# Kernel optimization log

Measured on AMD Instinct MI355X. Metric: run time of the kernel, lower is better.

Reference implementation:

```python
import jax, jax.numpy as jnp
import numpy as np

N_NODES = 100000
N_EDGES = 3200000
C, H, F = 512, 256, 64


def spmm(edge_row, edge_col, edge_val, Z):
    # (A @ Z)[i] = sum over edges e with row[e]==i of val[e] * Z[col[e]]
    msgs = edge_val[:, None] * Z[edge_col]  # [E, d]
    return jax.ops.segment_sum(msgs, edge_row, num_segments=N_NODES)


def setup_inputs() -> dict:
    key = jax.random.key(0)
    k1, k2, k3, k4, k5, k6, k7 = jax.random.split(key, 7)
    X = jax.random.normal(k1, (N_NODES, C), dtype=jnp.float32)
    edge_row = jax.random.randint(k2, (N_EDGES,), 0, N_NODES, dtype=jnp.int32)
    edge_col = jax.random.randint(k3, (N_EDGES,), 0, N_NODES, dtype=jnp.int32)
    edge_val = jax.random.uniform(k4, (N_EDGES,), dtype=jnp.float32)
    W0 = jax.random.normal(k5, (C, H), dtype=jnp.float32) * (C ** -0.5)
    Wh1 = jax.random.normal(k6, (H, H), dtype=jnp.float32) * (H ** -0.5)
    W1 = jax.random.normal(k7, (H, F), dtype=jnp.float32) * (H ** -0.5)
    return {"X": X, "edge_row": edge_row, "edge_col": edge_col,
            "edge_val": edge_val, "W0": W0, "Wh1": Wh1, "W1": W1}


def reference(X, edge_row, edge_col, edge_val, W0, Wh1, W1):
    # layer 0: relu(A @ (X W0))   (dropout=0 -> identity)
    Z = jax.nn.relu(spmm(edge_row, edge_col, edge_val, X @ W0))
    # hidden layers (num_layers - 2 = 1)
    Z = jax.nn.relu(spmm(edge_row, edge_col, edge_val, Z @ Wh1))
    # output layer: softmax(A @ (Z W1), axis=-1)
    Z = jax.nn.softmax(spmm(edge_row, edge_col, edge_val, Z @ W1), axis=-1)
    return Z
```

## Files before the change

### kernel.cpp

```cpp
#include <hip/hip_runtime.h>
#include <cstdint>
#include <cstddef>


#define SCAN_B 1024

typedef __attribute__((ext_vector_type(8))) short short8_t;
typedef __attribute__((ext_vector_type(4))) short short4_t;
typedef __attribute__((ext_vector_type(4))) float f32x4;

__device__ __forceinline__ short bf16_hi(float x) {
    union { float f; unsigned u; } c; c.f = x;
    return (short)(c.u >> 16);
}
__device__ __forceinline__ float bf16_f32(short h) {
    union { float f; unsigned u; } c; c.u = ((unsigned)(unsigned short)h) << 16;
    return c.f;
}

__device__ __forceinline__ void gload_lds16(const void* g, void* l) {
    __builtin_amdgcn_global_load_lds(
        (const __attribute__((address_space(1))) void*)g,
        (__attribute__((address_space(3))) void*)l, 16, 0, 0);
}


__global__ void count_rows_k(const int* __restrict__ row, int* __restrict__ deg, int E) {
    int e = blockIdx.x * blockDim.x + threadIdx.x;
    if (e < E) atomicAdd(&deg[row[e]], 1);
}

__global__ __launch_bounds__(SCAN_B) void scan1_k(const int* __restrict__ deg,
                                                  int* __restrict__ part,
                                                  int* __restrict__ bsum, int n) {
    __shared__ int buf[SCAN_B];
    int tid = threadIdx.x;
    int i = blockIdx.x * SCAN_B + tid;
    int v = (i < n) ? ((deg[i] + 3) & ~3) : 0;
    buf[tid] = v;
    __syncthreads();
    for (int off = 1; off < SCAN_B; off <<= 1) {
        int y = (tid >= off) ? buf[tid - off] : 0;
        __syncthreads();
        buf[tid] += y;
        __syncthreads();
    }
    if (i < n) part[i] = buf[tid] - v;
    if (tid == SCAN_B - 1) bsum[blockIdx.x] = buf[tid];
}

__global__ __launch_bounds__(128) void scan2_k(int* __restrict__ bsum, int nb) {
    __shared__ int buf[128];
    int tid = threadIdx.x;
    int v = (tid < nb) ? bsum[tid] : 0;
    buf[tid] = v;
    __syncthreads();
    for (int off = 1; off < 128; off <<= 1) {
        int y = (tid >= off) ? buf[tid - off] : 0;
        __syncthreads();
        buf[tid] += y;
        __syncthreads();
    }
    if (tid < nb) bsum[tid] = buf[tid] - v;
    if (tid == nb - 1) bsum[nb] = buf[tid];
}

__global__ __launch_bounds__(SCAN_B) void scan3_k(int* __restrict__ rowptr,
                                                  const int* __restrict__ bsum,
                                                  int* __restrict__ cursor, int n, int nb) {
    int i = blockIdx.x * SCAN_B + threadIdx.x;
    if (i < n) {
        int v = rowptr[i] + bsum[blockIdx.x];
        rowptr[i] = v;
        cursor[i] = v;
    }
    if (i == 0) rowptr[n] = bsum[nb];
}

__global__ void scatter_k(const int* __restrict__ row, const int* __restrict__ col,
                          const float* __restrict__ val, int* __restrict__ cursor,
                          int2* __restrict__ ecv, int E) {
    int e = blockIdx.x * blockDim.x + threadIdx.x;
    if (e < E) {
        int r = row[e];
        int p = atomicAdd(&cursor[r], 1);
        ecv[p] = make_int2(col[e], __float_as_int(val[e]));
    }
}


__global__ void split_w_k(const float* __restrict__ W, short* __restrict__ Bhl,
                          int K, int M) {
    int i = blockIdx.x * 256 + threadIdx.x;
    if (i >= K * M) return;
    int k = i / M, m = i - k * M;
    float x = W[i];
    short hi = bf16_hi(x);
    float r = x - bf16_f32(hi);
    short lo = bf16_hi(r);
    int g = k >> 3, j = k & 7;
    Bhl[(size_t)m * (2 * K) + 16 * g + j] = hi;
    Bhl[(size_t)m * (2 * K) + 16 * g + 8 + j] = lo;
}


template <int K, int BN, int NWR, int NWC, bool AF32>
__global__ __launch_bounds__(256) void gemm_hl(const void* __restrict__ Av,
                                               const short* __restrict__ Bhl,
                                               short* __restrict__ ZQ,
                                               float* __restrict__ scl, int N) {
    constexpr int BM = 64 * NWR;
    constexpr int NF = BN / NWC / 16;
    __shared__ short Ald[BM * 64];
    __shared__ short Bld[BN * 64];

    const int tid = threadIdx.x, lane = tid & 63, w = tid >> 6;
    const int wr = w / NWC, wc = w % NWC;
    const int row0 = blockIdx.x * BM;
    const int l8 = lane >> 3;
    const int sx = (lane & 7) ^ l8;

    f32x4 acc[4][NF] = {};

    for (int k0 = 0; k0 < K; k0 += 32) {
        if constexpr (AF32) {
            const float* A = (const float*)Av;
            int row = tid >> 2, q = tid & 3;
            int gr = row0 + row;
            float4 x0 = make_float4(0.f, 0.f, 0.f, 0.f), x1 = x0;
            if (gr < N) {
                x0 = *(const float4*)&A[(size_t)gr * K + k0 + q * 8];
                x1 = *(const float4*)&A[(size_t)gr * K + k0 + q * 8 + 4];
            }
            float f[8] = {x0.x, x0.y, x0.z, x0.w, x1.x, x1.y, x1.z, x1.w};
            short8_t hi, lo;
#pragma unroll
            for (int j = 0; j < 8; ++j) {
                short hh = bf16_hi(f[j]);
                hi[j] = hh;
                lo[j] = bf16_hi(f[j] - bf16_f32(hh));
            }
            int key = row & 7;
            *(short8_t*)&Ald[row * 64 + ((2 * q) ^ key) * 8] = hi;
            *(short8_t*)&Ald[row * 64 + ((2 * q + 1) ^ key) * 8] = lo;
        } else {
            const short* Ahl = (const short*)Av;
            for (int ch = w; ch < BM / 8; ch += 4)
                gload_lds16(Ahl + (size_t)(row0 + ch * 8 + l8) * (2 * K) + 2 * k0 + sx * 8,
                            &Ald[ch * 512]);
        }
        for (int ch = w; ch < BN / 8; ch += 4)
            gload_lds16(Bhl + (size_t)(ch * 8 + l8) * (2 * K) + 2 * k0 + sx * 8,
                        &Bld[ch * 512]);
        __syncthreads();

        const int sH = (lane >> 4) * 2, sL = sH + 1;
        short8_t ah[4], al[4];
#pragma unroll
        for (int m = 0; m < 4; ++m) {
            int rl = wr * 64 + m * 16 + (lane & 15);
            int key = rl & 7;
            ah[m] = *(const short8_t*)&Ald[rl * 64 + (sH ^ key) * 8];
            al[m] = *(const short8_t*)&Ald[rl * 64 + (sL ^ key) * 8];
        }
#pragma unroll
        for (int n = 0; n < NF; ++n) {
            int cl = wc * (BN / NWC) + n * 16 + (lane & 15);
            int key = cl & 7;
            short8_t bh = *(const short8_t*)&Bld[cl * 64 + (sH ^ key) * 8];
            short8_t bl = *(const short8_t*)&Bld[cl * 64 + (sL ^ key) * 8];
#pragma unroll
            for (int m = 0; m < 4; ++m) {
                acc[m][n] = __builtin_amdgcn_mfma_f32_16x16x32_bf16(ah[m], bh, acc[m][n], 0, 0, 0);
                acc[m][n] = __builtin_amdgcn_mfma_f32_16x16x32_bf16(ah[m], bl, acc[m][n], 0, 0, 0);
                acc[m][n] = __builtin_amdgcn_mfma_f32_16x16x32_bf16(al[m], bh, acc[m][n], 0, 0, 0);
            }
        }
        __syncthreads();
    }

    const int lg = lane >> 4, lc = lane & 15;
    float* maxb = (float*)Ald;
    float rmax[4][4];
#pragma unroll
    for (int m = 0; m < 4; ++m)
#pragma unroll
        for (int r = 0; r < 4; ++r) {
            float v = 0.f;
#pragma unroll
            for (int n = 0; n < NF; ++n) v = fmaxf(v, fabsf(acc[m][n][r]));
#pragma unroll
            for (int o = 8; o >= 1; o >>= 1) v = fmaxf(v, __shfl_xor(v, o));
            rmax[m][r] = v;
        }
    if constexpr (NWC > 1) {
        if (lc == 0)
#pragma unroll
            for (int m = 0; m < 4; ++m)
#pragma unroll
                for (int r = 0; r < 4; ++r)
                    maxb[(wr * 64 + m * 16 + lg * 4 + r) * NWC + wc] = rmax[m][r];
        __syncthreads();
    }
#pragma unroll
    for (int m = 0; m < 4; ++m)
#pragma unroll
        for (int r = 0; r < 4; ++r) {
            int rl = wr * 64 + m * 16 + lg * 4 + r;
            float v = rmax[m][r];
            if constexpr (NWC > 1) {
                v = maxb[rl * NWC];
#pragma unroll
                for (int q = 1; q < NWC; ++q) v = fmaxf(v, maxb[rl * NWC + q]);
            }
            int grow = row0 + rl;
            if (grow < N) {
                float inv = (v > 0.f) ? 32767.f / v : 0.f;
                if (lc == 0 && wc == 0) scl[grow] = v * (1.f / 32767.f);
#pragma unroll
                for (int n = 0; n < NF; ++n)
                    ZQ[(size_t)grow * BN + wc * (BN / NWC) + n * 16 + lc] =
                        (short)rintf(acc[m][n][r] * inv);
            }
        }
}


__global__ __launch_bounds__(256) void spmm_agg256_k(const int* __restrict__ rowptr,
                                                     const int2* __restrict__ ecv,
                                                     const short* __restrict__ Q,
                                                     const float* __restrict__ scl,
                                                     short* __restrict__ Zhl, int N) {
    int row = blockIdx.x * 4 + (threadIdx.x >> 6);
    if (row >= N) return;
    int lane = threadIdx.x & 63;
    int s = rowptr[row], e = rowptr[row + 1];
    const short4_t* Qv = (const short4_t*)Q;
    f32x4 acc = {0.f, 0.f, 0.f, 0.f};
    for (int i = s; i < e; i += 4) {
        int4 a = *(const int4*)(ecv + i);
        int4 b = *(const int4*)(ecv + i + 2);
        float w0 = __int_as_float(a.y) * scl[a.x];
        float w1 = __int_as_float(a.w) * scl[a.z];
        float w2 = __int_as_float(b.y) * scl[b.x];
        float w3 = __int_as_float(b.w) * scl[b.z];
        short4_t q0 = Qv[(size_t)a.x * 64 + lane];
        short4_t q1 = Qv[(size_t)a.z * 64 + lane];
        short4_t q2 = Qv[(size_t)b.x * 64 + lane];
        short4_t q3 = Qv[(size_t)b.z * 64 + lane];
#pragma unroll
        for (int j = 0; j < 4; ++j) {
            acc[j] = fmaf(w0, (float)q0[j], acc[j]);
            acc[j] = fmaf(w1, (float)q1[j], acc[j]);
            acc[j] = fmaf(w2, (float)q2[j], acc[j]);
            acc[j] = fmaf(w3, (float)q3[j], acc[j]);
        }
    }
    short4_t hi, lo;
#pragma unroll
    for (int j = 0; j < 4; ++j) {
        float r = fmaxf(acc[j], 0.f);
        short h = bf16_hi(r);
        hi[j] = h;
        lo[j] = bf16_hi(r - bf16_f32(h));
    }
    size_t base = (size_t)row * 512 + (lane >> 1) * 16 + (lane & 1) * 4;
    *(short4_t*)&Zhl[base] = hi;
    *(short4_t*)&Zhl[base + 8] = lo;
}

__global__ __launch_bounds__(256) void spmm_softmax64_k(const int* __restrict__ rowptr,
                                                        const int2* __restrict__ ecv,
                                                        const short* __restrict__ Q,
                                                        const float* __restrict__ scl,
                                                        float* __restrict__ out, int N) {
    int row = blockIdx.x * 4 + (threadIdx.x >> 6);
    if (row >= N) return;
    int lane = threadIdx.x & 63;
    int s = rowptr[row], e = rowptr[row + 1];
    float acc = 0.f;
    for (int i = s; i < e; i += 4) {
        int4 a = *(const int4*)(ecv + i);
        int4 b = *(const int4*)(ecv + i + 2);
        float w0 = __int_as_float(a.y) * scl[a.x];
        float w1 = __int_as_float(a.w) * scl[a.z];
        float w2 = __int_as_float(b.y) * scl[b.x];
        float w3 = __int_as_float(b.w) * scl[b.z];
        float z0 = (float)Q[(size_t)a.x * 64 + lane];
        float z1 = (float)Q[(size_t)a.z * 64 + lane];
        float z2 = (float)Q[(size_t)b.x * 64 + lane];
        float z3 = (float)Q[(size_t)b.z * 64 + lane];
        acc = fmaf(w0, z0, acc);
        acc = fmaf(w1, z1, acc);
        acc = fmaf(w2, z2, acc);
        acc = fmaf(w3, z3, acc);
    }
    float m = acc;
#pragma unroll
    for (int o = 32; o >= 1; o >>= 1) m = fmaxf(m, __shfl_xor(m, o));
    float p = __expf(acc - m);
    float ssum = p;
#pragma unroll
    for (int o = 32; o >= 1; o >>= 1) ssum += __shfl_xor(ssum, o);
    out[(size_t)row * 64 + lane] = p / ssum;
}


extern "C" void kernel_launch(void* const* d_in, const int* in_sizes, int n_in,
                              void* d_out, int out_size, void* d_ws, size_t ws_size,
                              hipStream_t stream) {
    const float* X        = (const float*)d_in[0];
    const int*   edge_row = (const int*)d_in[1];
    const int*   edge_col = (const int*)d_in[2];
    const float* edge_val = (const float*)d_in[3];
    const float* W0       = (const float*)d_in[4];
    const float* Wh1      = (const float*)d_in[5];
    const float* W1       = (const float*)d_in[6];

    const int C = 512, H = 256, F = 64;
    const int N = in_sizes[0] / C;
    const int E = in_sizes[1];
    const int EPAD = E + 4 * N + 64;

    size_t off = 0;
    auto alloc = [&](size_t bytes) -> void* {
        void* p = (char*)d_ws + off;
        off += (bytes + 255) & ~(size_t)255;
        return p;
    };
    short* Zhl    = (short*)alloc((size_t)N * 2 * H * sizeof(short));
    short* ZQ     = (short*)alloc((size_t)N * H * sizeof(short));
    float* scl    = (float*)alloc((size_t)N * sizeof(float));
    int*   deg    = (int*)alloc((size_t)N * sizeof(int));
    int*   rowptr = (int*)alloc((size_t)(N + 1) * sizeof(int));
    int*   cursor = (int*)alloc((size_t)N * sizeof(int));
    int*   bsum   = (int*)alloc(129 * sizeof(int));
    int2*  ecv    = (int2*)alloc((size_t)EPAD * sizeof(int2));
    short* Bhl0   = (short*)alloc((size_t)H * 2 * C * sizeof(short));
    short* Bhl1   = (short*)alloc((size_t)H * 2 * H * sizeof(short));
    short* Bhl2   = (short*)alloc((size_t)F * 2 * H * sizeof(short));
    (void)ws_size;

    hipMemsetAsync(deg, 0, (size_t)N * sizeof(int), stream);
    hipMemsetAsync(ecv, 0, (size_t)EPAD * sizeof(int2), stream);
    count_rows_k<<<(E + 255) / 256, 256, 0, stream>>>(edge_row, deg, E);
    int nb = (N + SCAN_B - 1) / SCAN_B;
    scan1_k<<<nb, SCAN_B, 0, stream>>>(deg, rowptr, bsum, N);
    scan2_k<<<1, 128, 0, stream>>>(bsum, nb);
    scan3_k<<<nb, SCAN_B, 0, stream>>>(rowptr, bsum, cursor, N, nb);
    scatter_k<<<(E + 255) / 256, 256, 0, stream>>>(edge_row, edge_col, edge_val,
                                                   cursor, ecv, E);

    split_w_k<<<(C * H + 255) / 256, 256, 0, stream>>>(W0, Bhl0, C, H);
    split_w_k<<<(H * H + 255) / 256, 256, 0, stream>>>(Wh1, Bhl1, H, H);
    split_w_k<<<(H * F + 255) / 256, 256, 0, stream>>>(W1, Bhl2, H, F);

    const int g64  = (N + 63) / 64;
    const int g128 = (N + 127) / 128;
    const int rg   = (N + 3) / 4;

    gemm_hl<512, 256, 1, 4, true><<<g64, 256, 0, stream>>>(X, Bhl0, ZQ, scl, N);
    spmm_agg256_k<<<rg, 256, 0, stream>>>(rowptr, ecv, ZQ, scl, Zhl, N);
    gemm_hl<256, 256, 1, 4, false><<<g64, 256, 0, stream>>>(Zhl, Bhl1, ZQ, scl, N);
    spmm_agg256_k<<<rg, 256, 0, stream>>>(rowptr, ecv, ZQ, scl, Zhl, N);
    gemm_hl<256, 64, 2, 2, false><<<g128, 256, 0, stream>>>(Zhl, Bhl2, ZQ, scl, N);
    spmm_softmax64_k<<<rg, 256, 0, stream>>>(rowptr, ecv, ZQ, scl,
                                             (float*)d_out, N);
}
```

Measured before the change: 1.136 ms.

## Double-buffer LDS tiles in split-bf16 GEMM to overlap loads with MFMA

The GEMM kernel now keeps two LDS buffers for the A and B tiles. It prefetches tile t+1, via global-to-LDS loads or register loads for fp32 A, while running the MFMAs on tile t, then writes the converted fp32 A after the compute. This removes one barrier per k-step and hides global load latency behind the matrix work. In exchange it doubles LDS use, which may lower occupancy, and adds register pressure for the fp32 prefetch.

```diff
diff --git a/kernel.cpp b/kernel.cpp
--- a/kernel.cpp
+++ b/kernel.cpp
@@ -111,8 +111,9 @@
                                                float* __restrict__ scl, int N) {
     constexpr int BM = 64 * NWR;
     constexpr int NF = BN / NWC / 16;
-    __shared__ short Ald[BM * 64];
-    __shared__ short Bld[BN * 64];
+    constexpr int NT = K / 32;
+    __shared__ short Ald[2][BM * 64];
+    __shared__ short Bld[2][BN * 64];
 
     const int tid = threadIdx.x, lane = tid & 63, w = tid >> 6;
     const int wr = w / NWC, wc = w % NWC;
@@ -120,39 +121,64 @@
     const int l8 = lane >> 3;
     const int sx = (lane & 7) ^ l8;
 
+    const short* Ahl = (const short*)Av;
+    const float* Af  = (const float*)Av;
+    const int arow = tid >> 2, aq = tid & 3;
+    const int akey = arow & 7;
+
     f32x4 acc[4][NF] = {};
 
-    for (int k0 = 0; k0 < K; k0 += 32) {
-        if constexpr (AF32) {
-            const float* A = (const float*)Av;
-            int row = tid >> 2, q = tid & 3;
-            int gr = row0 + row;
-            float4 x0 = make_float4(0.f, 0.f, 0.f, 0.f), x1 = x0;
-            if (gr < N) {
-                x0 = *(const float4*)&A[(size_t)gr * K + k0 + q * 8];
-                x1 = *(const float4*)&A[(size_t)gr * K + k0 + q * 8 + 4];
-            }
-            float f[8] = {x0.x, x0.y, x0.z, x0.w, x1.x, x1.y, x1.z, x1.w};
-            short8_t hi, lo;
-#pragma unroll
-            for (int j = 0; j < 8; ++j) {
-                short hh = bf16_hi(f[j]);
-                hi[j] = hh;
-                lo[j] = bf16_hi(f[j] - bf16_f32(hh));
-            }
-            int key = row & 7;
-            *(short8_t*)&Ald[row * 64 + ((2 * q) ^ key) * 8] = hi;
-            *(short8_t*)&Ald[row * 64 + ((2 * q + 1) ^ key) * 8] = lo;
-        } else {
-            const short* Ahl = (const short*)Av;
-            for (int ch = w; ch < BM / 8; ch += 4)
-                gload_lds16(Ahl + (size_t)(row0 + ch * 8 + l8) * (2 * K) + 2 * k0 + sx * 8,
-                            &Ald[ch * 512]);
-        }
+    auto stageB = [&](int t, int b) {
+#pragma unroll
         for (int ch = w; ch < BN / 8; ch += 4)
-            gload_lds16(Bhl + (size_t)(ch * 8 + l8) * (2 * K) + 2 * k0 + sx * 8,
-                        &Bld[ch * 512]);
-        __syncthreads();
+            gload_lds16(Bhl + (size_t)(ch * 8 + l8) * (2 * K) + (size_t)t * 64 + sx * 8,
+                        &Bld[b][ch * 512]);
+    };
+    auto stageAg = [&](int t, int b) {
+#pragma unroll
+        for (int ch = w; ch < BM / 8; ch += 4)
+            gload_lds16(Ahl + (size_t)(row0 + ch * 8 + l8) * (2 * K) + (size_t)t * 64 + sx * 8,
+                        &Ald[b][ch * 512]);
+    };
+    auto loadAf = [&](int t, float4& x0, float4& x1) {
+        int gr = row0 + arow;
+        x0 = make_float4(0.f, 0.f, 0.f, 0.f); x1 = x0;
+        if (gr < N) {
+            x0 = *(const float4*)&Af[(size_t)gr * K + t * 32 + aq * 8];
+            x1 = *(const float4*)&Af[(size_t)gr * K + t * 32 + aq * 8 + 4];
+        }
+    };
+    auto writeAf = [&](int b, float4 x0, float4 x1) {
+        float f[8] = {x0.x, x0.y, x0.z, x0.w, x1.x, x1.y, x1.z, x1.w};
+        short8_t hi, lo;
+#pragma unroll
+        for (int j = 0; j < 8; ++j) {
+            short hh = bf16_hi(f[j]);
+            hi[j] = hh;
+            lo[j] = bf16_hi(f[j] - bf16_f32(hh));
+        }
+        *(short8_t*)&Ald[b][arow * 64 + ((2 * aq) ^ akey) * 8] = hi;
+        *(short8_t*)&Ald[b][arow * 64 + ((2 * aq + 1) ^ akey) * 8] = lo;
+    };
+
+    if constexpr (AF32) {
+        float4 x0, x1;
+        loadAf(0, x0, x1);
+        writeAf(0, x0, x1);
+    } else {
+        stageAg(0, 0);
+    }
+    stageB(0, 0);
+    __syncthreads();
+
+    for (int t = 0; t < NT; ++t) {
+        const int cur = t & 1, nxt = cur ^ 1;
+        float4 px0, px1;
+        if (t + 1 < NT) {
+            if constexpr (AF32) loadAf(t + 1, px0, px1);
+            else                stageAg(t + 1, nxt);
+            stageB(t + 1, nxt);
+        }
 
         const int sH = (lane >> 4) * 2, sL = sH + 1;
         short8_t ah[4], al[4];
@@ -160,15 +186,15 @@
         for (int m = 0; m < 4; ++m) {
             int rl = wr * 64 + m * 16 + (lane & 15);
             int key = rl & 7;
-            ah[m] = *(const short8_t*)&Ald[rl * 64 + (sH ^ key) * 8];
-            al[m] = *(const short8_t*)&Ald[rl * 64 + (sL ^ key) * 8];
+            ah[m] = *(const short8_t*)&Ald[cur][rl * 64 + (sH ^ key) * 8];
+            al[m] = *(const short8_t*)&Ald[cur][rl * 64 + (sL ^ key) * 8];
         }
 #pragma unroll
         for (int n = 0; n < NF; ++n) {
             int cl = wc * (BN / NWC) + n * 16 + (lane & 15);
             int key = cl & 7;
-            short8_t bh = *(const short8_t*)&Bld[cl * 64 + (sH ^ key) * 8];
-            short8_t bl = *(const short8_t*)&Bld[cl * 64 + (sL ^ key) * 8];
+            short8_t bh = *(const short8_t*)&Bld[cur][cl * 64 + (sH ^ key) * 8];
+            short8_t bl = *(const short8_t*)&Bld[cur][cl * 64 + (sL ^ key) * 8];
 #pragma unroll
             for (int m = 0; m < 4; ++m) {
                 acc[m][n] = __builtin_amdgcn_mfma_f32_16x16x32_bf16(ah[m], bh, acc[m][n], 0, 0, 0);
@@ -176,11 +202,14 @@
                 acc[m][n] = __builtin_amdgcn_mfma_f32_16x16x32_bf16(al[m], bh, acc[m][n], 0, 0, 0);
             }
         }
+        if constexpr (AF32) {
+            if (t + 1 < NT) writeAf(nxt, px0, px1);
+        }
         __syncthreads();
     }
 
     const int lg = lane >> 4, lc = lane & 15;
-    float* maxb = (float*)Ald;
+    float* maxb = (float*)&Ald[0][0];
     float rmax[4][4];
 #pragma unroll
     for (int m = 0; m < 4; ++m)
```

New measurement: 1.168 ms. 2.9% more time.
